# Kernel tuning notes

Measured on AMD Instinct MI355X. Metric: run time of the kernel, lower is better.

## Reference

```python
import jax, jax.numpy as jnp
import numpy as np

ATT_WIDTH = 64  # local attention width, history_only=False
MASK_PENALTY = 10000.0


def setup_inputs() -> dict:
    key = jax.random.key(0)
    ks = jax.random.split(key, 4)
    B, L, D, U = 2, 1024, 256, 64
    x = jax.random.normal(ks[0], (B, L, D), dtype=jnp.float32)
    Wt = jax.random.normal(ks[1], (D, U), dtype=jnp.float32) * (1.0 / np.sqrt(D))
    Wx = jax.random.normal(ks[2], (D, U), dtype=jnp.float32) * (1.0 / np.sqrt(D))
    bh = jnp.zeros((U,), dtype=jnp.float32)
    Wa = jax.random.normal(ks[3], (U, 1), dtype=jnp.float32) * (1.0 / np.sqrt(U))
    ba = jnp.zeros((1,), dtype=jnp.float32)
    return {"x": x, "Wt": Wt, "Wx": Wx, "bh": bh, "Wa": Wa, "ba": ba}


def reference(x, Wt, Wx, bh, Wa, ba):
    B, L, D = x.shape
    # additive emission: e[b,i,j] = tanh(x_i Wt + x_j Wx + bh) . wa + ba
    q = jnp.einsum('bld,du->blu', x, Wt)  # [B,L,U]
    k = jnp.einsum('bld,du->blu', x, Wx)  # [B,L,U]
    h = jnp.tanh(q[:, :, None, :] + k[:, None, :, :] + bh)  # [B,L,L,U]
    e = jnp.einsum('biju,u->bij', h, Wa[:, 0]) + ba[0]  # [B,L,L]
    # local-width band mask (history_only=False -> centered window)
    idx = jnp.arange(L)
    lower = idx - ATT_WIDTH // 2          # [L]
    upper = lower + ATT_WIDTH             # [L]
    band = (lower[:, None] <= idx[None, :]) & (idx[None, :] < upper[:, None])
    e = e - MASK_PENALTY * (1.0 - band.astype(e.dtype))
    a = jax.nn.softmax(e, axis=-1)        # [B,L,L]
    v = jnp.einsum('bij,bjd->bid', a, x)  # [B,L,D]
    return v
```

## Files before the change

### kernel.cpp

```cpp
#include <hip/hip_runtime.h>


#define LSEQ  1024
#define DDIM  256
#define UDIM  64
#define NROWS 2048
#define RPB   4
#define JMAX  68

__global__ __launch_bounds__(256) void qk_kernel(
    const float* __restrict__ x, const float* __restrict__ Wt,
    const float* __restrict__ Wx, const float* __restrict__ bh,
    float* __restrict__ q, float* __restrict__ k) {
  int t = threadIdx.x;
  int u = t & 63;
  int sel = (t >> 6) & 1;
  int r0 = blockIdx.x * 8 + (t >> 7) * 4;
  const float* __restrict__ W = sel ? Wx : Wt;
  const float4* __restrict__ x0 = (const float4*)(x + (r0 + 0) * DDIM);
  const float4* __restrict__ x1 = (const float4*)(x + (r0 + 1) * DDIM);
  const float4* __restrict__ x2 = (const float4*)(x + (r0 + 2) * DDIM);
  const float4* __restrict__ x3 = (const float4*)(x + (r0 + 3) * DDIM);
  float a0 = 0.f, a1 = 0.f, a2 = 0.f, a3 = 0.f;
#pragma unroll 4
  for (int d4 = 0; d4 < DDIM / 4; ++d4) {
    const float* wp = W + d4 * 4 * UDIM + u;
    float w0 = wp[0], w1 = wp[64], w2 = wp[128], w3 = wp[192];
    float4 v0 = x0[d4], v1 = x1[d4], v2 = x2[d4], v3 = x3[d4];
    a0 += v0.x * w0 + v0.y * w1 + v0.z * w2 + v0.w * w3;
    a1 += v1.x * w0 + v1.y * w1 + v1.z * w2 + v1.w * w3;
    a2 += v2.x * w0 + v2.y * w1 + v2.z * w2 + v2.w * w3;
    a3 += v3.x * w0 + v3.y * w1 + v3.z * w2 + v3.w * w3;
  }
  float* __restrict__ dst = sel ? k : q;
  float bias = sel ? 0.f : bh[u];
  dst[(r0 + 0) * UDIM + u] = a0 + bias;
  dst[(r0 + 1) * UDIM + u] = a1 + bias;
  dst[(r0 + 2) * UDIM + u] = a2 + bias;
  dst[(r0 + 3) * UDIM + u] = a3 + bias;
}

__device__ __forceinline__ float tanh_fast(float v) {
  float t = __expf(-2.f * v);
  return 2.f * __builtin_amdgcn_rcpf(1.f + t) - 1.f;
}

__device__ __forceinline__ float bcast(float v, int l) {
  return __uint_as_float(__builtin_amdgcn_readlane(__float_as_uint(v), l));
}

__global__ __launch_bounds__(256) void attn_kernel(
    const float* __restrict__ x, const float* __restrict__ q,
    const float* __restrict__ k, const float* __restrict__ Wa,
    float* __restrict__ out) {
  __shared__ float k_lds[JMAX][UDIM + 1];
  __shared__ float a_lds[RPB][JMAX];

  int t = threadIdx.x;
  int lane = t & 63;
  int wid = t >> 6;
  int g0 = blockIdx.x * RPB;
  int b = g0 >> 10;
  int i0 = g0 & (LSEQ - 1);
  int jbase = max(0, i0 - 32);
  int jend = min(LSEQ, i0 + RPB - 1 + 32);
  int jcount = jend - jbase;

  for (int jj = wid; jj < jcount; jj += 4)
    k_lds[jj][lane] = k[(b * LSEQ + jbase + jj) * UDIM + lane];
  for (int z = t; z < RPB * JMAX; z += 256) ((float*)a_lds)[z] = 0.f;
  float qv = q[(g0 + wid) * UDIM + lane];
  float wv = Wa[lane];
  __syncthreads();

  int i = i0 + wid;
  int lo = max(0, i - 32);
  int hi = min(LSEQ, i + 32);
  int off = lo - jbase;
  bool valid = (lo + lane) < hi;
  const float* __restrict__ kr = &k_lds[off + lane][0];
  float e = 0.f;
#pragma unroll
  for (int u = 0; u < UDIM; ++u)
    e += bcast(wv, u) * tanh_fast(bcast(qv, u) + kr[u]);

  float m = valid ? e : -3.4e38f;
#pragma unroll
  for (int o = 32; o >= 1; o >>= 1) m = fmaxf(m, __shfl_xor(m, o));
  float p = valid ? __expf(e - m) : 0.f;
  float s = p;
#pragma unroll
  for (int o = 32; o >= 1; o >>= 1) s += __shfl_xor(s, o);
  a_lds[wid][off + lane] = p * __builtin_amdgcn_rcpf(s);
  __syncthreads();

  const float* __restrict__ xq = x + b * LSEQ * DDIM + wid * 64 + lane;
  float c0 = 0.f, c1 = 0.f, c2 = 0.f, c3 = 0.f;
  int nch = (jcount + 3) >> 2;
  for (int ch = 0; ch < nch; ++ch) {
    int jj = ch * 4;
    float4 A0 = *(const float4*)&a_lds[0][jj];
    float4 A1 = *(const float4*)&a_lds[1][jj];
    float4 A2 = *(const float4*)&a_lds[2][jj];
    float4 A3 = *(const float4*)&a_lds[3][jj];
    int j0 = jbase + jj;
    float xv0 = xq[min(j0 + 0, jend - 1) * DDIM];
    float xv1 = xq[min(j0 + 1, jend - 1) * DDIM];
    float xv2 = xq[min(j0 + 2, jend - 1) * DDIM];
    float xv3 = xq[min(j0 + 3, jend - 1) * DDIM];
    c0 += A0.x * xv0 + A0.y * xv1 + A0.z * xv2 + A0.w * xv3;
    c1 += A1.x * xv0 + A1.y * xv1 + A1.z * xv2 + A1.w * xv3;
    c2 += A2.x * xv0 + A2.y * xv1 + A2.z * xv2 + A2.w * xv3;
    c3 += A3.x * xv0 + A3.y * xv1 + A3.z * xv2 + A3.w * xv3;
  }
  float* __restrict__ ob = out + g0 * DDIM + wid * 64 + lane;
  ob[0 * DDIM] = c0;
  ob[1 * DDIM] = c1;
  ob[2 * DDIM] = c2;
  ob[3 * DDIM] = c3;
}

extern "C" void kernel_launch(void* const* d_in, const int* in_sizes, int n_in,
                              void* d_out, int out_size, void* d_ws, size_t ws_size,
                              hipStream_t stream) {
  const float* x  = (const float*)d_in[0];
  const float* Wt = (const float*)d_in[1];
  const float* Wx = (const float*)d_in[2];
  const float* bh = (const float*)d_in[3];
  const float* Wa = (const float*)d_in[4];
  float* out = (float*)d_out;

  float* q = (float*)d_ws;
  float* k = q + NROWS * UDIM;

  qk_kernel<<<NROWS / 8, 256, 0, stream>>>(x, Wt, Wx, bh, q, k);
  attn_kernel<<<NROWS / RPB, 256, 0, stream>>>(x, q, k, Wa, out);
}
```

Baseline: 90.83 us.

## Fold tanh scaling into q/k projection and use exp2 with LDS broadcasts

The projection kernel now pre-multiplies q and k by -2·log2(e), so the inner loop can call exp2 directly with no per-element multiply. The tanh affine terms are hoisted: the sum of w·rcp(1+t) is accumulated, then doubled and corrected by the sum of Wa once per row. The readlane broadcasts of q and Wa are replaced by float4 LDS reads. The qk kernel also processes 2 rows per thread instead of 4 across twice as many blocks.

New measurement: 89.26 us. About the same (-1.7%).

```diff
diff --git a/kernel.cpp b/kernel.cpp
--- a/kernel.cpp
+++ b/kernel.cpp
@@ -8,6 +8,14 @@
 #define RPB   4
 #define JMAX  68
 
+#if __has_builtin(__builtin_amdgcn_exp2f)
+#define EXPFN(x) __builtin_amdgcn_exp2f(x)
+#define PRESCALE -2.8853900817779268f
+#else
+#define EXPFN(x) __expf(x)
+#define PRESCALE -2.0f
+#endif
+
 __global__ __launch_bounds__(256) void qk_kernel(
     const float* __restrict__ x, const float* __restrict__ Wt,
     const float* __restrict__ Wx, const float* __restrict__ bh,
@@ -15,38 +23,23 @@
   int t = threadIdx.x;
   int u = t & 63;
   int sel = (t >> 6) & 1;
-  int r0 = blockIdx.x * 8 + (t >> 7) * 4;
+  int r0 = blockIdx.x * 4 + (t >> 7) * 2;
   const float* __restrict__ W = sel ? Wx : Wt;
   const float4* __restrict__ x0 = (const float4*)(x + (r0 + 0) * DDIM);
   const float4* __restrict__ x1 = (const float4*)(x + (r0 + 1) * DDIM);
-  const float4* __restrict__ x2 = (const float4*)(x + (r0 + 2) * DDIM);
-  const float4* __restrict__ x3 = (const float4*)(x + (r0 + 3) * DDIM);
-  float a0 = 0.f, a1 = 0.f, a2 = 0.f, a3 = 0.f;
-#pragma unroll 4
+  float a0 = 0.f, a1 = 0.f;
+#pragma unroll 8
   for (int d4 = 0; d4 < DDIM / 4; ++d4) {
     const float* wp = W + d4 * 4 * UDIM + u;
     float w0 = wp[0], w1 = wp[64], w2 = wp[128], w3 = wp[192];
-    float4 v0 = x0[d4], v1 = x1[d4], v2 = x2[d4], v3 = x3[d4];
+    float4 v0 = x0[d4], v1 = x1[d4];
     a0 += v0.x * w0 + v0.y * w1 + v0.z * w2 + v0.w * w3;
     a1 += v1.x * w0 + v1.y * w1 + v1.z * w2 + v1.w * w3;
-    a2 += v2.x * w0 + v2.y * w1 + v2.z * w2 + v2.w * w3;
-    a3 += v3.x * w0 + v3.y * w1 + v3.z * w2 + v3.w * w3;
   }
+  float bias = sel ? 0.f : bh[u];
   float* __restrict__ dst = sel ? k : q;
-  float bias = sel ? 0.f : bh[u];
-  dst[(r0 + 0) * UDIM + u] = a0 + bias;
-  dst[(r0 + 1) * UDIM + u] = a1 + bias;
-  dst[(r0 + 2) * UDIM + u] = a2 + bias;
-  dst[(r0 + 3) * UDIM + u] = a3 + bias;
-}
-
-__device__ __forceinline__ float tanh_fast(float v) {
-  float t = __expf(-2.f * v);
-  return 2.f * __builtin_amdgcn_rcpf(1.f + t) - 1.f;
-}
-
-__device__ __forceinline__ float bcast(float v, int l) {
-  return __uint_as_float(__builtin_amdgcn_readlane(__float_as_uint(v), l));
+  dst[(r0 + 0) * UDIM + u] = PRESCALE * (a0 + bias);
+  dst[(r0 + 1) * UDIM + u] = PRESCALE * (a1 + bias);
 }
 
 __global__ __launch_bounds__(256) void attn_kernel(
@@ -54,6 +47,8 @@
     const float* __restrict__ k, const float* __restrict__ Wa,
     float* __restrict__ out) {
   __shared__ float k_lds[JMAX][UDIM + 1];
+  __shared__ float qs[RPB][UDIM];
+  __shared__ float was[UDIM];
   __shared__ float a_lds[RPB][JMAX];
 
   int t = threadIdx.x;
@@ -68,9 +63,13 @@
 
   for (int jj = wid; jj < jcount; jj += 4)
     k_lds[jj][lane] = k[(b * LSEQ + jbase + jj) * UDIM + lane];
+  qs[wid][lane] = q[(g0 + wid) * UDIM + lane];
+  float wv = Wa[lane];
+  if (wid == 0) was[lane] = wv;
   for (int z = t; z < RPB * JMAX; z += 256) ((float*)a_lds)[z] = 0.f;
-  float qv = q[(g0 + wid) * UDIM + lane];
-  float wv = Wa[lane];
+  float swa = wv;
+#pragma unroll
+  for (int o = 32; o >= 1; o >>= 1) swa += __shfl_xor(swa, o);
   __syncthreads();
 
   int i = i0 + wid;
@@ -79,10 +78,21 @@
   int off = lo - jbase;
   bool valid = (lo + lane) < hi;
   const float* __restrict__ kr = &k_lds[off + lane][0];
-  float e = 0.f;
+  float e2 = 0.f;
 #pragma unroll
-  for (int u = 0; u < UDIM; ++u)
-    e += bcast(wv, u) * tanh_fast(bcast(qv, u) + kr[u]);
+  for (int u4 = 0; u4 < UDIM; u4 += 4) {
+    float4 q4 = *(const float4*)&qs[wid][u4];
+    float4 w4 = *(const float4*)&was[u4];
+    float t0 = EXPFN(q4.x + kr[u4 + 0]);
+    float t1 = EXPFN(q4.y + kr[u4 + 1]);
+    float t2 = EXPFN(q4.z + kr[u4 + 2]);
+    float t3 = EXPFN(q4.w + kr[u4 + 3]);
+    e2 += w4.x * __builtin_amdgcn_rcpf(1.f + t0);
+    e2 += w4.y * __builtin_amdgcn_rcpf(1.f + t1);
+    e2 += w4.z * __builtin_amdgcn_rcpf(1.f + t2);
+    e2 += w4.w * __builtin_amdgcn_rcpf(1.f + t3);
+  }
+  float e = 2.f * e2 - swa;
 
   float m = valid ? e : -3.4e38f;
 #pragma unroll
@@ -133,6 +143,6 @@
   float* q = (float*)d_ws;
   float* k = q + NROWS * UDIM;
 
-  qk_kernel<<<NROWS / 8, 256, 0, stream>>>(x, Wt, Wx, bh, q, k);
+  qk_kernel<<<NROWS / 4, 256, 0, stream>>>(x, Wt, Wx, bh, q, k);
   attn_kernel<<<NROWS / RPB, 256, 0, stream>>>(x, q, k, Wa, out);
 }
```
